# Kernel tuning notes

Measured on AMD Instinct MI355X. Metric: run time of the kernel, lower is better.

## Reference

```python
import jax, jax.numpy as jnp
import numpy as np

T, B, D, H_DIM = 1024, 64, 512, 512
SIGMA = 0.01


def setup_inputs() -> dict:
    key = jax.random.key(0)
    ks = jax.random.split(key, 9)
    inp = {
        "inputs": jax.random.normal(ks[0], (T, B, D), dtype=jnp.float32),
        "W_xi": jax.random.normal(ks[1], (D, H_DIM), dtype=jnp.float32) * SIGMA,
        "W_hi": jax.random.normal(ks[2], (H_DIM, H_DIM), dtype=jnp.float32) * SIGMA,
        "b_i": jnp.zeros((H_DIM,), dtype=jnp.float32),
        "W_xf": jax.random.normal(ks[3], (D, H_DIM), dtype=jnp.float32) * SIGMA,
        "W_hf": jax.random.normal(ks[4], (H_DIM, H_DIM), dtype=jnp.float32) * SIGMA,
        "b_f": jnp.zeros((H_DIM,), dtype=jnp.float32),
        "W_xo": jax.random.normal(ks[5], (D, H_DIM), dtype=jnp.float32) * SIGMA,
        "W_ho": jax.random.normal(ks[6], (H_DIM, H_DIM), dtype=jnp.float32) * SIGMA,
        "b_o": jnp.zeros((H_DIM,), dtype=jnp.float32),
        "W_xc": jax.random.normal(ks[7], (D, H_DIM), dtype=jnp.float32) * SIGMA,
        "W_hc": jax.random.normal(ks[8], (H_DIM, H_DIM), dtype=jnp.float32) * SIGMA,
        "b_c": jnp.zeros((H_DIM,), dtype=jnp.float32),
    }
    return inp


def reference(inputs, W_xi, W_hi, b_i, W_xf, W_hf, b_f,
              W_xo, W_ho, b_o, W_xc, W_hc, b_c):
    # inputs: [T, B, D]. Precompute input-to-gate projections in one big
    # batched GEMM per gate (same math as per-step X @ W_x + b).
    Xi = jnp.einsum('tbd,dh->tbh', inputs, W_xi) + b_i
    Xf = jnp.einsum('tbd,dh->tbh', inputs, W_xf) + b_f
    Xo = jnp.einsum('tbd,dh->tbh', inputs, W_xo) + b_o
    Xc = jnp.einsum('tbd,dh->tbh', inputs, W_xc) + b_c

    Bsz = inputs.shape[1]
    H0 = jnp.zeros((Bsz, W_hi.shape[0]), dtype=inputs.dtype)
    C0 = jnp.zeros((Bsz, W_hi.shape[0]), dtype=inputs.dtype)

    def step(carry, xs):
        H, C = carry
        xi, xf, xo, xc = xs
        I = jax.nn.sigmoid(xi + H @ W_hi)
        F = jax.nn.sigmoid(xf + H @ W_hf)
        O = jax.nn.sigmoid(xo + H @ W_ho)
        C_tilde = jnp.tanh(xc + H @ W_hc)
        C = F * C + I * C_tilde
        H = O * jnp.tanh(C)
        return (H, C), H

    (H, C), outputs = jax.lax.scan(step, (H0, C0), (Xi, Xf, Xo, Xc))
    # outputs: [T, B, H] stacked hidden states (torch returns a list of them)
    return outputs, (H, C)
```

## Files before the change

### kernel.cpp

```cpp
#include <hip/hip_runtime.h>
#include <hip/hip_bf16.h>
#include <stdint.h>


typedef float    f32x4  __attribute__((ext_vector_type(4)));
typedef short    s16x8  __attribute__((ext_vector_type(8)));
typedef unsigned short u16;
typedef u16      u16x4  __attribute__((ext_vector_type(4)));
typedef unsigned int u32;

#define TT 1024
#define BB 64
#define DD 512
#define HH 512
#define NG 2048
#define NTEAM 8
#define NSLOT 8
#define NLW 128

__device__ __forceinline__ u16 f2bf(float f) {
  __hip_bfloat16 h = __float2bfloat16(f);
  union { __hip_bfloat16 b; u16 u; } v; v.b = h; return v.u;
}
__device__ __forceinline__ float bf2f(u16 u) {
  union { unsigned int i; float f; } v; v.i = ((unsigned int)u) << 16; return v.f;
}
__device__ __forceinline__ float sig_fast(float x) {
  return 1.f / (1.f + __expf(-x));
}
__device__ __forceinline__ float tanh_fast(float x) {
  return 1.f - 2.f / (1.f + __expf(2.f * x));
}

__device__ __forceinline__ void gload_lds16(const u16* g, u16* l) {
  __builtin_amdgcn_global_load_lds(
      (const __attribute__((address_space(1))) unsigned int*)g,
      (__attribute__((address_space(3))) unsigned int*)l, 16, 0, 0);
}

__device__ __forceinline__ void st_plain(u32* p, u32 v) {
  asm volatile("global_store_dword %0, %1, off" :: "v"(p), "v"(v) : "memory");
}

__global__ void k_cast(const float* __restrict__ in, u16* __restrict__ out, long n) {
  long i = ((long)blockIdx.x * blockDim.x + threadIdx.x) * 4;
  if (i >= n) return;
  const float4 v = *(const float4*)(in + i);
  u16x4 o; o.x = f2bf(v.x); o.y = f2bf(v.y); o.z = f2bf(v.z); o.w = f2bf(v.w);
  *(u16x4*)(out + i) = o;
}

__global__ void k_pack(const float* __restrict__ Wxi, const float* __restrict__ Whi, const float* __restrict__ bi,
                       const float* __restrict__ Wxf, const float* __restrict__ Whf, const float* __restrict__ bfi,
                       const float* __restrict__ Wxo, const float* __restrict__ Who, const float* __restrict__ bo,
                       const float* __restrict__ Wxc, const float* __restrict__ Whc, const float* __restrict__ bc,
                       u16* __restrict__ WxT, u16* __restrict__ WhT, float* __restrict__ biasp)
{
  const int k = blockIdx.x;
  const float* Wx[4] = {Wxi, Wxf, Wxo, Wxc};
  const float* Wh[4] = {Whi, Whf, Who, Whc};
  for (int h = threadIdx.x; h < HH; h += blockDim.x) {
#pragma unroll
    for (int g = 0; g < 4; ++g) {
      const long n = h * 4 + g;
      WxT[n * DD + k] = f2bf(Wx[g][(long)k * HH + h]);
      WhT[n * HH + k] = f2bf(Wh[g][(long)k * HH + h]);
    }
  }
  if (k == 0) {
    const float* bp[4] = {bi, bfi, bo, bc};
    for (int n = threadIdx.x; n < NG; n += blockDim.x)
      biasp[n] = bp[n & 3][n >> 2];
  }
}

__global__ __launch_bounds__(256) void k_gemm_x(
    const u16* __restrict__ A, const u16* __restrict__ BT,
    const float* __restrict__ biasp, u16* __restrict__ X)
{
  __shared__ __align__(16) u16 As[128 * 64];
  __shared__ __align__(16) u16 Bs[128 * 64];
  const int tid = threadIdx.x;
  const int l = tid & 63;
  const int w = tid >> 6;
  const int wr = w >> 1, wc = w & 1;
  const long brow = (long)blockIdx.y * 128;
  const int  bcol = blockIdx.x * 128;
  const int  lr = l >> 3, lc = l & 7;
  const int  cl = l & 15, rg = l >> 4;

  f32x4 acc[4][4];
#pragma unroll
  for (int m = 0; m < 4; ++m)
#pragma unroll
    for (int n = 0; n < 4; ++n) acc[m][n] = (f32x4){0.f, 0.f, 0.f, 0.f};

  for (int k0 = 0; k0 < DD; k0 += 64) {
#pragma unroll
    for (int j = 0; j < 4; ++j) {
      const int sub = w * 4 + j;
      gload_lds16(A  + (brow + sub * 8 + lr) * DD + k0 + lc * 8, &As[sub * 512]);
      gload_lds16(BT + ((long)(bcol + sub * 8 + lr)) * DD + k0 + lc * 8, &Bs[sub * 512]);
    }
    __syncthreads();
#pragma unroll
    for (int kk = 0; kk < 2; ++kk) {
      s16x8 af[4], bfr[4];
#pragma unroll
      for (int m = 0; m < 4; ++m)
        af[m] = *(const s16x8*)&As[(wr * 64 + m * 16 + cl) * 64 + kk * 32 + rg * 8];
#pragma unroll
      for (int n = 0; n < 4; ++n)
        bfr[n] = *(const s16x8*)&Bs[(wc * 64 + n * 16 + cl) * 64 + kk * 32 + rg * 8];
#pragma unroll
      for (int m = 0; m < 4; ++m)
#pragma unroll
        for (int n = 0; n < 4; ++n)
          acc[m][n] = __builtin_amdgcn_mfma_f32_16x16x32_bf16(af[m], bfr[n], acc[m][n], 0, 0, 0);
    }
    __syncthreads();
  }
#pragma unroll
  for (int n = 0; n < 4; ++n) {
    const int col = bcol + wc * 64 + n * 16 + cl;
    const float bv = biasp[col];
#pragma unroll
    for (int m = 0; m < 4; ++m)
#pragma unroll
      for (int j = 0; j < 4; ++j) {
        const long row = brow + wr * 64 + m * 16 + rg * 4 + j;
        X[row * NG + col] = f2bf(acc[m][n][j] + bv);
      }
  }
}

__global__ __launch_bounds__(512, 2) void k_lstm(
    const u16* __restrict__ X, const u16* __restrict__ WhT,
    u16* __restrict__ Hh, float* __restrict__ Cst,
    float* __restrict__ dout, float* __restrict__ doutH, float* __restrict__ doutC,
    u32* __restrict__ ctl, u32* __restrict__ flags, int t0, int t1)
{
  __shared__ __align__(16) float pre[8][260];
  __shared__ int s_team, s_slot, s_mixed;
  const int tid = threadIdx.x;

  if (tid == 0) {
    u32 x;
    asm volatile("s_getreg_b32 %0, hwreg(HW_REG_XCC_ID)" : "=s"(x));
    x &= 7u;
    u32 r = __hip_atomic_fetch_add(&ctl[x], 1u, __ATOMIC_RELAXED, __HIP_MEMORY_SCOPE_AGENT);
    u32 p = 0;
    if (r >= NSLOT)
      p = __hip_atomic_fetch_add(&ctl[8], 1u, __ATOMIC_RELAXED, __HIP_MEMORY_SCOPE_AGENT);
    __hip_atomic_fetch_add(&ctl[9], 1u, __ATOMIC_RELAXED, __HIP_MEMORY_SCOPE_AGENT);
    while (__hip_atomic_load(&ctl[9], __ATOMIC_RELAXED, __HIP_MEMORY_SCOPE_AGENT) < (u32)NLW)
      __builtin_amdgcn_s_sleep(4);
    u32 c[8];
#pragma unroll
    for (int i = 0; i < 8; ++i)
      c[i] = __hip_atomic_load(&ctl[i], __ATOMIC_RELAXED, __HIP_MEMORY_SCOPE_AGENT);
    int team = -1, slot = 0;
    if (r < NSLOT) { team = (int)x; slot = (int)r; }
    else {
      u32 acc = 0;
      for (int tt = 0; tt < 8; ++tt) {
        u32 have = c[tt] < NSLOT ? c[tt] : NSLOT;
        u32 miss = NSLOT - have;
        if (team < 0 && p < acc + miss) { team = tt; slot = (int)(have + (p - acc)); }
        acc += miss;
      }
    }
    s_team = team; s_slot = slot;
    s_mixed = (team >= 0 && c[team] < NSLOT) ? 1 : 0;
  }
  __syncthreads();
  const int team = s_team, slot = s_slot, mixed = s_mixed;
  if (team < 0) return;

  const int l = tid & 63, wv = tid >> 6;
  const int cl = l & 15, rg = l >> 4;
  const int gcol0 = slot * 256 + wv * 32;

  s16x8 bfr[2][16];
#pragma unroll
  for (int nt = 0; nt < 2; ++nt)
#pragma unroll
    for (int ks = 0; ks < 16; ++ks)
      bfr[nt][ks] = *(const s16x8*)&WhT[(long)(gcol0 + nt * 16 + cl) * HH + ks * 32 + rg * 8];

  const int prow = tid >> 6;
  const int phl  = tid & 63;
  const int grow = team * 8 + prow;
  const int ghl  = slot * 64 + phl;

  float creg;
  if (t0 == 0) creg = 0.f; else creg = Cst[grow * HH + ghl];

  u32* myflag = &flags[(team * 8 + slot) * 32];

  for (int t = t0; t < t1; ++t) {
    const int s = t - t0;
    u16x4 xv = *(const u16x4*)&X[((long)s * BB + grow) * NG + slot * 256 + phl * 4];

    if (t > t0) {
      if (wv == 0) {
        const u32 tgt = (u32)t;
        u32 vv; unsigned long long b;
        do {
          vv = (l < NSLOT)
             ? __hip_atomic_load(&flags[(team * 8 + l) * 32], __ATOMIC_RELAXED, __HIP_MEMORY_SCOPE_AGENT)
             : tgt;
          b = __ballot(vv >= tgt);
        } while (b != ~0ULL);
      }
      __syncthreads();
    }

    f32x4 acc0 = (f32x4){0.f,0.f,0.f,0.f}, acc1 = (f32x4){0.f,0.f,0.f,0.f};
    if (t > 0) {
      const u16* Hp = Hh + (long)(t - 1) * BB * HH;
      s16x8 af[16];
#pragma unroll
      for (int ks = 0; ks < 16; ++ks) af[ks] = (s16x8){0,0,0,0,0,0,0,0};
      if (cl < 8) {
#pragma unroll
        for (int ks = 0; ks < 16; ++ks)
          af[ks] = *(const s16x8*)&Hp[(team * 8 + cl) * HH + ks * 32 + rg * 8];
      }
#pragma unroll
      for (int ks = 0; ks < 16; ++ks) {
        acc0 = __builtin_amdgcn_mfma_f32_16x16x32_bf16(af[ks], bfr[0][ks], acc0, 0, 0, 0);
        acc1 = __builtin_amdgcn_mfma_f32_16x16x32_bf16(af[ks], bfr[1][ks], acc1, 0, 0, 0);
      }
    }
    if (rg < 2) {
#pragma unroll
      for (int j = 0; j < 4; ++j) {
        pre[rg * 4 + j][wv * 32 + cl]      = acc0[j];
        pre[rg * 4 + j][wv * 32 + 16 + cl] = acc1[j];
      }
    }
    __syncthreads();

    f32x4 pv = *(const f32x4*)&pre[prow][phl * 4];
    const float pi = pv[0] + bf2f((u16)xv.x);
    const float pf = pv[1] + bf2f((u16)xv.y);
    const float po = pv[2] + bf2f((u16)xv.z);
    const float pc = pv[3] + bf2f((u16)xv.w);
    const float ig = sig_fast(pi);
    const float fg = sig_fast(pf);
    const float og = sig_fast(po);
    const float ct = tanh_fast(pc);
    creg = fg * creg + ig * ct;
    const float hv = og * tanh_fast(creg);
    const u16 hb = f2bf(hv);
    u16* hdst = &Hh[((long)t * BB + grow) * HH + ghl];
    if (!mixed) *hdst = hb;
    else asm volatile("global_store_short %0, %1, off sc1"
                      :: "v"(hdst), "v"((u32)hb) : "memory");

    asm volatile("s_waitcnt vmcnt(0)" ::: "memory");
    __syncthreads();
    if (tid == 0) {
      if (!mixed) st_plain(myflag, (u32)(t + 1));
      else __hip_atomic_store(myflag, (u32)(t + 1),
                              __ATOMIC_RELAXED, __HIP_MEMORY_SCOPE_AGENT);
    }
    dout[((long)t * BB + grow) * HH + ghl] = hv;
    if (t == TT - 1) {
      doutH[grow * HH + ghl] = hv;
      doutC[grow * HH + ghl] = creg;
    }
  }

  Cst[grow * HH + ghl] = creg;
}

extern "C" void kernel_launch(void* const* d_in, const int* in_sizes, int n_in,
                              void* d_out, int out_size, void* d_ws, size_t ws_size,
                              hipStream_t stream)
{
  const float* inputs = (const float*)d_in[0];
  const float* W_xi = (const float*)d_in[1];
  const float* W_hi = (const float*)d_in[2];
  const float* b_i  = (const float*)d_in[3];
  const float* W_xf = (const float*)d_in[4];
  const float* W_hf = (const float*)d_in[5];
  const float* b_f  = (const float*)d_in[6];
  const float* W_xo = (const float*)d_in[7];
  const float* W_ho = (const float*)d_in[8];
  const float* b_o  = (const float*)d_in[9];
  const float* W_xc = (const float*)d_in[10];
  const float* W_hc = (const float*)d_in[11];
  const float* b_c  = (const float*)d_in[12];
  float* out = (float*)d_out;
  char* ws = (char*)d_ws;

  size_t off = 0;
  auto walloc = [&](size_t sz) { size_t o = off; off = (off + sz + 255) & ~(size_t)255; return o; };
  const size_t o_inbf  = walloc((size_t)TT * BB * DD * 2);
  const size_t o_WxT   = walloc((size_t)NG * DD * 2);
  const size_t o_WhT   = walloc((size_t)NG * HH * 2);
  const size_t o_bias  = walloc((size_t)NG * 4);
  const size_t o_C     = walloc((size_t)BB * HH * 4);
  const size_t o_Hh    = walloc((size_t)TT * BB * HH * 2);
  const size_t o_ctl   = walloc(256);
  const size_t o_flags = walloc(8192);
  const size_t o_X     = off;

  const size_t bytes_per_step = (size_t)BB * NG * 2;
  long spc = (ws_size > o_X) ? (long)((ws_size - o_X) / bytes_per_step) : 0;
  if (spc > TT) spc = TT;
  spc &= ~1L;
  if (spc < 2) spc = 2;

  u16*   inbf  = (u16*)(ws + o_inbf);
  u16*   WxT   = (u16*)(ws + o_WxT);
  u16*   WhT   = (u16*)(ws + o_WhT);
  float* biasp = (float*)(ws + o_bias);
  u16*   Xbuf  = (u16*)(ws + o_X);
  u16*   Hh    = (u16*)(ws + o_Hh);
  float* Cst   = (float*)(ws + o_C);

  k_cast<<<dim3((TT * BB * DD) / 1024), dim3(256), 0, stream>>>(inputs, inbf, (long)TT * BB * DD);
  k_pack<<<dim3(DD), dim3(256), 0, stream>>>(W_xi, W_hi, b_i, W_xf, W_hf, b_f,
                                             W_xo, W_ho, b_o, W_xc, W_hc, b_c,
                                             WxT, WhT, biasp);

  float* doutH = out + (size_t)TT * BB * HH;
  float* doutC = doutH + (size_t)BB * HH;

  for (int t0 = 0; t0 < TT; t0 += (int)spc) {
    int t1 = t0 + (int)spc; if (t1 > TT) t1 = TT;
    const int rows = (t1 - t0) * BB;
    k_gemm_x<<<dim3(NG / 128, rows / 128), dim3(256), 0, stream>>>(
        inbf + (size_t)t0 * BB * DD, WxT, biasp, Xbuf);
    hipMemsetAsync(ws + o_ctl, 0, 256, stream);
    hipMemsetAsync(ws + o_flags, 0, 8192, stream);
    k_lstm<<<dim3(NLW), dim3(512), 0, stream>>>(
        Xbuf, WhT, Hh, Cst, out, doutH, doutC,
        (u32*)(ws + o_ctl), (u32*)(ws + o_flags), t0, t1);
  }
}
```

Baseline: 4.315 ms.

## Run input GEMM once and the recurrence in a single persistent launch

Drops the chunked loop that alternated input-projection GEMM and recurrent kernel launches, assuming the workspace can hold the full projected X tensor, and runs one GEMM followed by one k_lstm over all time steps. This removes the cell-state save/restore and the repeated launch/memset overhead. It also splits the MFMA accumulation into two independent chains to shorten dependency latency. It moves the output stores before the vmcnt wait and flag publish, and lowers launch bounds to one block per CU. Risk: it no longer checks ws_size, so a small workspace would overflow, and the output stores now sit on the per-step critical path before the flag release.

```diff
diff --git a/kernel.cpp b/kernel.cpp
--- a/kernel.cpp
+++ b/kernel.cpp
@@ -25,19 +25,14 @@
 __device__ __forceinline__ float bf2f(u16 u) {
   union { unsigned int i; float f; } v; v.i = ((unsigned int)u) << 16; return v.f;
 }
-__device__ __forceinline__ float sig_fast(float x) {
-  return 1.f / (1.f + __expf(-x));
-}
-__device__ __forceinline__ float tanh_fast(float x) {
-  return 1.f - 2.f / (1.f + __expf(2.f * x));
-}
+__device__ __forceinline__ float sig_fast(float x) { return 1.f / (1.f + __expf(-x)); }
+__device__ __forceinline__ float tanh_fast(float x) { return 1.f - 2.f / (1.f + __expf(2.f * x)); }
 
 __device__ __forceinline__ void gload_lds16(const u16* g, u16* l) {
   __builtin_amdgcn_global_load_lds(
       (const __attribute__((address_space(1))) unsigned int*)g,
       (__attribute__((address_space(3))) unsigned int*)l, 16, 0, 0);
 }
-
 __device__ __forceinline__ void st_plain(u32* p, u32 v) {
   asm volatile("global_store_dword %0, %1, off" :: "v"(p), "v"(v) : "memory");
 }
@@ -134,11 +129,11 @@
   }
 }
 
-__global__ __launch_bounds__(512, 2) void k_lstm(
+__global__ __launch_bounds__(512, 1) void k_lstm(
     const u16* __restrict__ X, const u16* __restrict__ WhT,
-    u16* __restrict__ Hh, float* __restrict__ Cst,
+    u16* __restrict__ Hh,
     float* __restrict__ dout, float* __restrict__ doutH, float* __restrict__ doutC,
-    u32* __restrict__ ctl, u32* __restrict__ flags, int t0, int t1)
+    u32* __restrict__ ctl, u32* __restrict__ flags)
 {
   __shared__ __align__(16) float pre[8][260];
   __shared__ int s_team, s_slot, s_mixed;
@@ -192,17 +187,13 @@
   const int phl  = tid & 63;
   const int grow = team * 8 + prow;
   const int ghl  = slot * 64 + phl;
-
-  float creg;
-  if (t0 == 0) creg = 0.f; else creg = Cst[grow * HH + ghl];
-
+  float creg = 0.f;
   u32* myflag = &flags[(team * 8 + slot) * 32];
 
-  for (int t = t0; t < t1; ++t) {
-    const int s = t - t0;
-    u16x4 xv = *(const u16x4*)&X[((long)s * BB + grow) * NG + slot * 256 + phl * 4];
-
-    if (t > t0) {
+  for (int t = 0; t < TT; ++t) {
+    u16x4 xv = *(const u16x4*)&X[((long)t * BB + grow) * NG + slot * 256 + phl * 4];
+
+    if (t > 0) {
       if (wv == 0) {
         const u32 tgt = (u32)t;
         u32 vv; unsigned long long b;
@@ -216,7 +207,8 @@
       __syncthreads();
     }
 
-    f32x4 acc0 = (f32x4){0.f,0.f,0.f,0.f}, acc1 = (f32x4){0.f,0.f,0.f,0.f};
+    f32x4 a0a = (f32x4){0.f,0.f,0.f,0.f}, a0b = (f32x4){0.f,0.f,0.f,0.f};
+    f32x4 a1a = (f32x4){0.f,0.f,0.f,0.f}, a1b = (f32x4){0.f,0.f,0.f,0.f};
     if (t > 0) {
       const u16* Hp = Hh + (long)(t - 1) * BB * HH;
       s16x8 af[16];
@@ -228,11 +220,14 @@
           af[ks] = *(const s16x8*)&Hp[(team * 8 + cl) * HH + ks * 32 + rg * 8];
       }
 #pragma unroll
-      for (int ks = 0; ks < 16; ++ks) {
-        acc0 = __builtin_amdgcn_mfma_f32_16x16x32_bf16(af[ks], bfr[0][ks], acc0, 0, 0, 0);
-        acc1 = __builtin_amdgcn_mfma_f32_16x16x32_bf16(af[ks], bfr[1][ks], acc1, 0, 0, 0);
-      }
-    }
+      for (int ks = 0; ks < 16; ks += 2) {
+        a0a = __builtin_amdgcn_mfma_f32_16x16x32_bf16(af[ks],     bfr[0][ks],     a0a, 0, 0, 0);
+        a1a = __builtin_amdgcn_mfma_f32_16x16x32_bf16(af[ks],     bfr[1][ks],     a1a, 0, 0, 0);
+        a0b = __builtin_amdgcn_mfma_f32_16x16x32_bf16(af[ks + 1], bfr[0][ks + 1], a0b, 0, 0, 0);
+        a1b = __builtin_amdgcn_mfma_f32_16x16x32_bf16(af[ks + 1], bfr[1][ks + 1], a1b, 0, 0, 0);
+      }
+    }
+    const f32x4 acc0 = a0a + a0b, acc1 = a1a + a1b;
     if (rg < 2) {
 #pragma unroll
       for (int j = 0; j < 4; ++j) {
@@ -259,21 +254,18 @@
     else asm volatile("global_store_short %0, %1, off sc1"
                       :: "v"(hdst), "v"((u32)hb) : "memory");
 
+    dout[((long)t * BB + grow) * HH + ghl] = hv;
+    if (t == TT - 1) {
+      doutH[grow * HH + ghl] = hv;
+      doutC[grow * HH + ghl] = creg;
+    }
     asm volatile("s_waitcnt vmcnt(0)" ::: "memory");
     __syncthreads();
     if (tid == 0) {
       if (!mixed) st_plain(myflag, (u32)(t + 1));
-      else __hip_atomic_store(myflag, (u32)(t + 1),
-                              __ATOMIC_RELAXED, __HIP_MEMORY_SCOPE_AGENT);
-    }
-    dout[((long)t * BB + grow) * HH + ghl] = hv;
-    if (t == TT - 1) {
-      doutH[grow * HH + ghl] = hv;
-      doutC[grow * HH + ghl] = creg;
-    }
-  }
-
-  Cst[grow * HH + ghl] = creg;
+      else __hip_atomic_store(myflag, (u32)(t + 1), __ATOMIC_RELAXED, __HIP_MEMORY_SCOPE_AGENT);
+    }
+  }
 }
 
 extern "C" void kernel_launch(void* const* d_in, const int* in_sizes, int n_in,
@@ -302,17 +294,10 @@
   const size_t o_WxT   = walloc((size_t)NG * DD * 2);
   const size_t o_WhT   = walloc((size_t)NG * HH * 2);
   const size_t o_bias  = walloc((size_t)NG * 4);
-  const size_t o_C     = walloc((size_t)BB * HH * 4);
   const size_t o_Hh    = walloc((size_t)TT * BB * HH * 2);
   const size_t o_ctl   = walloc(256);
   const size_t o_flags = walloc(8192);
-  const size_t o_X     = off;
-
-  const size_t bytes_per_step = (size_t)BB * NG * 2;
-  long spc = (ws_size > o_X) ? (long)((ws_size - o_X) / bytes_per_step) : 0;
-  if (spc > TT) spc = TT;
-  spc &= ~1L;
-  if (spc < 2) spc = 2;
+  const size_t o_X     = walloc((size_t)TT * BB * NG * 2);
 
   u16*   inbf  = (u16*)(ws + o_inbf);
   u16*   WxT   = (u16*)(ws + o_WxT);
@@ -320,25 +305,21 @@
   float* biasp = (float*)(ws + o_bias);
   u16*   Xbuf  = (u16*)(ws + o_X);
   u16*   Hh    = (u16*)(ws + o_Hh);
-  float* Cst   = (float*)(ws + o_C);
 
   k_cast<<<dim3((TT * BB * DD) / 1024), dim3(256), 0, stream>>>(inputs, inbf, (long)TT * BB * DD);
   k_pack<<<dim3(DD), dim3(256), 0, stream>>>(W_xi, W_hi, b_i, W_xf, W_hf, b_f,
                                              W_xo, W_ho, b_o, W_xc, W_hc, b_c,
                                              WxT, WhT, biasp);
+  k_gemm_x<<<dim3(NG / 128, (TT * BB) / 128), dim3(256), 0, stream>>>(
+      inbf, WxT, biasp, Xbuf);
 
   float* doutH = out + (size_t)TT * BB * HH;
   float* doutC = doutH + (size_t)BB * HH;
 
-  for (int t0 = 0; t0 < TT; t0 += (int)spc) {
-    int t1 = t0 + (int)spc; if (t1 > TT) t1 = TT;
-    const int rows = (t1 - t0) * BB;
-    k_gemm_x<<<dim3(NG / 128, rows / 128), dim3(256), 0, stream>>>(
-        inbf + (size_t)t0 * BB * DD, WxT, biasp, Xbuf);
-    hipMemsetAsync(ws + o_ctl, 0, 256, stream);
-    hipMemsetAsync(ws + o_flags, 0, 8192, stream);
-    k_lstm<<<dim3(NLW), dim3(512), 0, stream>>>(
-        Xbuf, WhT, Hh, Cst, out, doutH, doutC,
-        (u32*)(ws + o_ctl), (u32*)(ws + o_flags), t0, t1);
-  }
-}
+  hipMemsetAsync(ws + o_ctl, 0, 256, stream);
+  hipMemsetAsync(ws + o_flags, 0, 8192, stream);
+
+  k_lstm<<<dim3(NLW), dim3(512), 0, stream>>>(
+      Xbuf, WhT, Hh, out, doutH, doutC,
+      (u32*)(ws + o_ctl), (u32*)(ws + o_flags));
+}
```

After: 4.290 ms. No clear change (-0.6%).
